# Performance work log

Hardware: AMD Instinct MI355X
Metric: run time of the kernel (lower is better)

The kernel has to match this reference:

```python
import jax, jax.numpy as jnp
import numpy as np

H_IMG, W_IMG = 1024, 1280
MAX_ITER = 3
DAMPING = 1e-6
DIST_THR = 0.2
NORM_THR = float(np.cos(np.deg2rad(20.0)))


def setup_inputs() -> dict:
    key = jax.random.key(0)
    k1, k2, k3, k4 = jax.random.split(key, 4)
    H, W = H_IMG, W_IMG
    fx = fy = 1000.0
    cx, cy = (W - 1) / 2.0, (H - 1) / 2.0
    K = jnp.array([[fx, 0.0, cx], [0.0, fy, cy], [0.0, 0.0, 1.0]], dtype=jnp.float32)
    # backproject a random depth map so vertex maps are geometrically consistent with K
    depth = 0.5 + 2.5 * jax.random.uniform(k1, (H, W), dtype=jnp.float32)
    vv, uu = jnp.meshgrid(jnp.arange(H, dtype=jnp.float32), jnp.arange(W, dtype=jnp.float32), indexing='ij')
    vertex_t0 = jnp.stack([(uu - cx) / fx * depth, (vv - cy) / fy * depth, depth], axis=-1)
    n = jax.random.normal(k2, (H, W, 3), dtype=jnp.float32) * 0.1 + jnp.array([0.0, 0.0, -1.0], jnp.float32)
    normal_t0 = n / jnp.linalg.norm(n, axis=-1, keepdims=True)
    # frame 1 = slightly perturbed frame 0 (realistic small-motion ICP)
    vertex_t1 = vertex_t0 + 0.002 * jax.random.normal(k3, (H, W, 3), dtype=jnp.float32)
    n1 = normal_t0 + 0.01 * jax.random.normal(k4, (H, W, 3), dtype=jnp.float32)
    normal_t1 = n1 / jnp.linalg.norm(n1, axis=-1, keepdims=True)
    pose10 = jnp.eye(4, dtype=jnp.float32).at[:3, 3].set(jnp.array([0.005, -0.003, 0.002], jnp.float32))
    return {
        'pose10': pose10,
        'vertex_t0': vertex_t0.astype(jnp.float32),
        'vertex_t1': vertex_t1.astype(jnp.float32),
        'normal_t0': normal_t0.astype(jnp.float32),
        'normal_t1': normal_t1.astype(jnp.float32),
        'K': K,
    }


def _skew3(w):
    o = jnp.zeros((), w.dtype)
    return jnp.array([[o, -w[2], w[1]], [w[2], o, -w[0]], [-w[1], w[0], o]])


def _exp_se3(xi):
    w, v = xi[:3], xi[3:6]
    wh = _skew3(w)
    wh2 = wh @ wh
    theta = jnp.linalg.norm(w)
    eps = 1e-8
    ts = jnp.maximum(theta, eps)  # safe denominator
    sin_t, cos_t = jnp.sin(ts), jnp.cos(ts)
    eye3 = jnp.eye(3, dtype=xi.dtype)
    e_w_big = eye3 + wh * (sin_t / ts) + wh2 * ((1.0 - cos_t) / ts ** 2)
    j_big = eye3 + ((1.0 - cos_t) / ts ** 2) * wh + ((ts - sin_t) / ts ** 3) * wh2
    small = theta <= eps
    e_w = jnp.where(small, eye3, e_w_big)
    j = jnp.where(small, eye3, j_big)
    return jnp.eye(4, dtype=xi.dtype).at[:3, :3].set(e_w).at[:3, 3].set(j @ v)


def _warp_nearest(feat, u, v):
    # grid_sample(mode='nearest', padding='border', align_corners=True) with
    # the module's normalization reduces to nearest-pixel gather at (v,u), clamped.
    H, W, _ = feat.shape
    ui = jnp.clip(jnp.round(u), 0, W - 1).astype(jnp.int32)
    vi = jnp.clip(jnp.round(v), 0, H - 1).astype(jnp.int32)
    return feat[vi, ui]  # (H,W,C)


def _icp_step(pose, vertex0, vertex1, normal0, normal1, mask0, K):
    R, t = pose[:3, :3], pose[:3, 3]
    H, W, _ = vertex0.shape
    p = vertex0 @ R.T + t          # vertex0_to1, (H,W,3)
    n0 = normal0 @ R.T             # normal0_to1
    fx, fy, cx, cy = K[0, 0], K[1, 1], K[0, 2], K[1, 2]
    z = p[..., 2]
    u = p[..., 0] / z * fx + cx
    v = p[..., 1] / z * fy + cy
    inview = (u > 0) & (u < W - 1) & (v > 0) & (v < H - 1)
    rv1 = _warp_nearest(vertex1, u, v)
    rn1 = _warp_nearest(normal1, u, v)
    mask1 = rv1[..., -1] > 0.0
    diff = p - rv1
    normal_ok = jnp.sum(n0 * rn1, axis=-1) > NORM_THR
    res = jnp.sum(rn1 * diff, axis=-1)           # (H,W)
    # -n^T skew(p) == cross(p, n)
    J = jnp.concatenate([jnp.cross(p, rn1), rn1], axis=-1)  # (H,W,6)
    occ = (~inview) | (jnp.linalg.norm(diff, axis=-1) > DIST_THR)
    invalid = occ | (~mask0) | (~mask1) | (~normal_ok)
    J = jnp.where(invalid[..., None], 0.0, J).reshape(-1, 6)
    r = jnp.where(invalid, 0.0, res).reshape(-1)
    JtJ = J.T @ J                                 # (6,6)
    JtR = J.T @ r                                 # (6,)
    Hm = JtJ + jnp.trace(JtJ) * DAMPING * jnp.eye(6, dtype=JtJ.dtype)
    xi = -(jnp.linalg.inv(Hm) @ JtR)
    return _exp_se3(xi) @ pose, ~invalid


def reference(pose10, vertex_t0, vertex_t1, normal_t0, normal_t1, K):
    mask0 = vertex_t0[..., -1] > 0.0
    pose = pose10
    valid = None
    for _ in range(MAX_ITER):
        pose, valid = _icp_step(pose, vertex_t0, vertex_t1, normal_t0, normal_t1, mask0, K)
    H, W = vertex_t0.shape[:2]
    valid_ratio = valid.astype(jnp.float32).sum() / H / W
    return pose, valid_ratio
```

## Files before the change

### kernel.cpp

```cpp
#include <hip/hip_runtime.h>
#include <math.h>

#define H_IMG 1024
#define W_IMG 1280
#define NPIX (H_IMG * W_IMG)
#define NQUAD (NPIX / 4)
#define RBLOCKS 256
#define RTPB 256
#define QPT (NQUAD / (RBLOCKS * RTPB))
#define NACC 28
#define NREP 8
#define NORM_THR 0.93969262f
#define DIST_THR2 0.04f
#define DAMPING 1e-6

#define ACC_DOUBLES (NREP * NACC * 8)

__global__ __launch_bounds__(256) void icp_init(const float* __restrict__ pose_in,
                                                double* __restrict__ ws) {
    const int i = threadIdx.x;
    if (i < 16) ws[i] = (double)pose_in[i];
    for (int k = i; k < ACC_DOUBLES; k += 256) ws[16 + k] = 0.0;
    if (i == 0) *(unsigned*)(ws + 16 + ACC_DOUBLES) = 0u;
}

__device__ void solve_and_update(const double* tot, double* pose_ws,
                                 float* out, int write_out) {
    double JtJ[6][6];
    {
        int k = 0;
        for (int i = 0; i < 6; ++i)
            for (int j = i; j < 6; ++j) { JtJ[i][j] = tot[k]; JtJ[j][i] = tot[k]; ++k; }
    }
    double tr = 0.0;
    for (int i = 0; i < 6; ++i) tr += JtJ[i][i];

    double A[6][7];
    for (int i = 0; i < 6; ++i) {
        for (int j = 0; j < 6; ++j) A[i][j] = JtJ[i][j] + (i == j ? tr * DAMPING : 0.0);
        A[i][6] = -tot[21 + i];
    }
    for (int c = 0; c < 6; ++c) {
        int piv = c; double mx = fabs(A[c][c]);
        for (int r = c + 1; r < 6; ++r) {
            double ar = fabs(A[r][c]);
            if (ar > mx) { mx = ar; piv = r; }
        }
        if (piv != c) for (int j = 0; j < 7; ++j) { double tmp = A[c][j]; A[c][j] = A[piv][j]; A[piv][j] = tmp; }
        double d = A[c][c]; if (d == 0.0) d = 1e-30;
        for (int r = c + 1; r < 6; ++r) {
            double f = A[r][c] / d;
            for (int j = c; j < 7; ++j) A[r][j] -= f * A[c][j];
        }
    }
    double xi[6];
    for (int i = 5; i >= 0; --i) {
        double s = A[i][6];
        for (int j = i + 1; j < 6; ++j) s -= A[i][j] * xi[j];
        double d = A[i][i]; if (d == 0.0) d = 1e-30;
        xi[i] = s / d;
    }

    const double w0 = xi[0], w1 = xi[1], w2 = xi[2];
    const double v0 = xi[3], v1 = xi[4], v2 = xi[5];
    double wh[3][3] = { {0.0, -w2, w1}, {w2, 0.0, -w0}, {-w1, w0, 0.0} };
    double wh2[3][3];
    for (int i = 0; i < 3; ++i)
        for (int j = 0; j < 3; ++j) {
            double s = 0.0;
            for (int k = 0; k < 3; ++k) s += wh[i][k] * wh[k][j];
            wh2[i][j] = s;
        }
    const double theta = sqrt(w0 * w0 + w1 * w1 + w2 * w2);
    const double eps = 1e-8;
    const double ts = (theta > eps) ? theta : eps;
    const double st = sin(ts), ct = cos(ts);
    const double cA = st / ts;
    const double cB = (1.0 - ct) / (ts * ts);
    const double cC = (ts - st) / (ts * ts * ts);
    const bool small = (theta <= eps);

    double ew[3][3], Jm[3][3];
    for (int i = 0; i < 3; ++i)
        for (int j = 0; j < 3; ++j) {
            double eye = (i == j) ? 1.0 : 0.0;
            ew[i][j] = small ? eye : (eye + cA * wh[i][j] + cB * wh2[i][j]);
            Jm[i][j] = small ? eye : (eye + cB * wh[i][j] + cC * wh2[i][j]);
        }
    double Jv[3];
    for (int i = 0; i < 3; ++i) Jv[i] = Jm[i][0] * v0 + Jm[i][1] * v1 + Jm[i][2] * v2;

    double T[16] = { ew[0][0], ew[0][1], ew[0][2], Jv[0],
                     ew[1][0], ew[1][1], ew[1][2], Jv[1],
                     ew[2][0], ew[2][1], ew[2][2], Jv[2],
                     0.0, 0.0, 0.0, 1.0 };
    double P[16];
    for (int i = 0; i < 16; ++i) P[i] = pose_ws[i];
    double NP[16];
    for (int i = 0; i < 4; ++i)
        for (int j = 0; j < 4; ++j) {
            double s = 0.0;
            for (int k = 0; k < 4; ++k) s += T[i * 4 + k] * P[k * 4 + j];
            NP[i * 4 + j] = s;
        }
    for (int i = 0; i < 16; ++i) pose_ws[i] = NP[i];

    if (write_out) {
        for (int i = 0; i < 16; ++i) out[i] = (float)NP[i];
        out[16] = (float)(tot[27] / (double)NPIX);
    }
}

__global__ __launch_bounds__(RTPB) void icp_fused(
    const float* __restrict__ vert0, const float* __restrict__ vert1,
    const float* __restrict__ norm0, const float* __restrict__ norm1,
    const float* __restrict__ Kmat, double* __restrict__ ws,
    float* __restrict__ out, int write_out)
{
    const double* pose = ws;
    double* acc = ws + 16;
    unsigned* counter = (unsigned*)(ws + 16 + ACC_DOUBLES);

    const float R00 = (float)pose[0],  R01 = (float)pose[1],  R02 = (float)pose[2],  t0 = (float)pose[3];
    const float R10 = (float)pose[4],  R11 = (float)pose[5],  R12 = (float)pose[6],  t1 = (float)pose[7];
    const float R20 = (float)pose[8],  R21 = (float)pose[9],  R22 = (float)pose[10], t2 = (float)pose[11];
    const float fx = Kmat[0], cx = Kmat[2], fy = Kmat[4], cy = Kmat[5];

    float a[NACC];
#pragma unroll
    for (int k = 0; k < NACC; ++k) a[k] = 0.0f;

    auto do_pixel = [&](float v0x, float v0y, float v0z,
                        float n0x, float n0y, float n0z) {
        const float px = R00 * v0x + R01 * v0y + R02 * v0z + t0;
        const float py = R10 * v0x + R11 * v0y + R12 * v0z + t1;
        const float pz = R20 * v0x + R21 * v0y + R22 * v0z + t2;
        const float nrx = R00 * n0x + R01 * n0y + R02 * n0z;
        const float nry = R10 * n0x + R11 * n0y + R12 * n0z;
        const float nrz = R20 * n0x + R21 * n0y + R22 * n0z;

        const float u = px / pz * fx + cx;
        const float v = py / pz * fy + cy;
        const bool inview = (u > 0.0f) && (u < (float)(W_IMG - 1)) &&
                            (v > 0.0f) && (v < (float)(H_IMG - 1));

        const float uf = fminf(fmaxf(rintf(u), 0.0f), (float)(W_IMG - 1));
        const float vf = fminf(fmaxf(rintf(v), 0.0f), (float)(H_IMG - 1));
        const int wbase = ((int)vf * W_IMG + (int)uf) * 3;

        const float r1x = vert1[wbase], r1y = vert1[wbase + 1], r1z = vert1[wbase + 2];
        const float m1x = norm1[wbase], m1y = norm1[wbase + 1], m1z = norm1[wbase + 2];

        const float dx = px - r1x, dy = py - r1y, dz = pz - r1z;
        const bool mask0 = v0z > 0.0f;
        const bool mask1 = r1z > 0.0f;
        const bool normal_ok = (nrx * m1x + nry * m1y + nrz * m1z) > NORM_THR;
        const float d2 = dx * dx + dy * dy + dz * dz;
        const bool occ = (!inview) || (d2 > DIST_THR2);
        const bool valid = (!occ) && mask0 && mask1 && normal_ok;

        if (valid) {
            const float res = m1x * dx + m1y * dy + m1z * dz;
            float J[6];
            J[0] = py * m1z - pz * m1y;
            J[1] = pz * m1x - px * m1z;
            J[2] = px * m1y - py * m1x;
            J[3] = m1x; J[4] = m1y; J[5] = m1z;
            int k = 0;
#pragma unroll
            for (int i = 0; i < 6; ++i)
#pragma unroll
                for (int j = i; j < 6; ++j) a[k++] += J[i] * J[j];
#pragma unroll
            for (int i = 0; i < 6; ++i) a[21 + i] += J[i] * res;
            a[27] += 1.0f;
        }
    };

    const int tid0 = blockIdx.x * RTPB + threadIdx.x;
    const float4* v0q = (const float4*)vert0;
    const float4* n0q = (const float4*)norm0;

#pragma unroll
    for (int i = 0; i < QPT; ++i) {
        const int q = tid0 + i * (RBLOCKS * RTPB);
        const float4 A0 = v0q[q * 3 + 0], A1 = v0q[q * 3 + 1], A2 = v0q[q * 3 + 2];
        const float4 B0 = n0q[q * 3 + 0], B1 = n0q[q * 3 + 1], B2 = n0q[q * 3 + 2];
        do_pixel(A0.x, A0.y, A0.z, B0.x, B0.y, B0.z);
        do_pixel(A0.w, A1.x, A1.y, B0.w, B1.x, B1.y);
        do_pixel(A1.z, A1.w, A2.x, B1.z, B1.w, B2.x);
        do_pixel(A2.y, A2.z, A2.w, B2.y, B2.z, B2.w);
    }

#pragma unroll
    for (int k = 0; k < NACC; ++k) {
        float val = a[k];
        for (int off = 32; off > 0; off >>= 1) val += __shfl_down(val, off, 64);
        a[k] = val;
    }

    __shared__ float sh[4][NACC];
    const int lane = threadIdx.x & 63;
    const int wid  = threadIdx.x >> 6;
    if (lane == 0) {
#pragma unroll
        for (int k = 0; k < NACC; ++k) sh[wid][k] = a[k];
    }
    __syncthreads();

    const unsigned tid = threadIdx.x;
    const int rep = blockIdx.x & (NREP - 1);
    if (tid < NACC) {
        double s = (double)sh[0][tid] + (double)sh[1][tid] +
                   (double)sh[2][tid] + (double)sh[3][tid];
        atomicAdd(&acc[(rep * NACC + (int)tid) * 8], s);
        __threadfence();
    }
    __syncthreads();

    __shared__ bool amLast;
    if (tid == 0) {
        unsigned prev = atomicAdd(counter, 1u);
        amLast = (prev == gridDim.x - 1);
    }
    __syncthreads();

    if (amLast) {
        __shared__ double tot[NACC];
        if (tid < NACC) {
            double s = 0.0;
            for (int r = 0; r < NREP; ++r)
                s += atomicAdd(&acc[(r * NACC + (int)tid) * 8], 0.0);
            tot[tid] = s;
            for (int r = 0; r < NREP; ++r)
                atomicExch((unsigned long long*)&acc[(r * NACC + (int)tid) * 8], 0ull);
        }
        if (tid == 0) atomicExch(counter, 0u);
        __syncthreads();
        if (tid == 0) solve_and_update(tot, ws, out, write_out);
    }
}

extern "C" void kernel_launch(void* const* d_in, const int* in_sizes, int n_in,
                              void* d_out, int out_size, void* d_ws, size_t ws_size,
                              hipStream_t stream) {
    const float* pose10 = (const float*)d_in[0];
    const float* vert0  = (const float*)d_in[1];
    const float* vert1  = (const float*)d_in[2];
    const float* norm0  = (const float*)d_in[3];
    const float* norm1  = (const float*)d_in[4];
    const float* Kmat   = (const float*)d_in[5];
    float* out = (float*)d_out;
    double* ws = (double*)d_ws;

    icp_init<<<1, 256, 0, stream>>>(pose10, ws);
    for (int it = 0; it < 3; ++it) {
        icp_fused<<<RBLOCKS, RTPB, 0, stream>>>(vert0, vert1, norm0, norm1,
                                                Kmat, ws, out, it == 2 ? 1 : 0);
    }
}
```

Measured before the change: 194.4 us.

## Prefetch next quad and batch gathers; replace atomic accumulators with per-block partials

The per-pixel loop now handles four pixels at a time. It computes all projections first, then issues all gather loads, and prefetches the next quad's vertex and normal data so memory latency overlaps with the accumulation math. The contended double atomicAdds into 8 replicas are replaced by per-block partial stores. The last block then reduces those partials in parallel, using 224 threads followed by a shared-memory tree step. This trades more register pressure (launch_bounds min-blocks set to 1) for more memory-level parallelism and fewer global atomics.

```diff
diff --git a/kernel.cpp b/kernel.cpp
--- a/kernel.cpp
+++ b/kernel.cpp
@@ -9,19 +9,18 @@
 #define RTPB 256
 #define QPT (NQUAD / (RBLOCKS * RTPB))
 #define NACC 28
-#define NREP 8
 #define NORM_THR 0.93969262f
 #define DIST_THR2 0.04f
 #define DAMPING 1e-6
 
-#define ACC_DOUBLES (NREP * NACC * 8)
+#define PART_DOUBLES (RBLOCKS * NACC)
 
 __global__ __launch_bounds__(256) void icp_init(const float* __restrict__ pose_in,
                                                 double* __restrict__ ws) {
     const int i = threadIdx.x;
     if (i < 16) ws[i] = (double)pose_in[i];
-    for (int k = i; k < ACC_DOUBLES; k += 256) ws[16 + k] = 0.0;
-    if (i == 0) *(unsigned*)(ws + 16 + ACC_DOUBLES) = 0u;
+    for (int k = i; k < PART_DOUBLES; k += 256) ws[16 + k] = 0.0;
+    if (i == 0) *(unsigned*)(ws + 16 + PART_DOUBLES) = 0u;
 }
 
 __device__ void solve_and_update(const double* tot, double* pose_ws,
@@ -111,15 +110,15 @@
     }
 }
 
-__global__ __launch_bounds__(RTPB) void icp_fused(
+__global__ __launch_bounds__(RTPB, 1) void icp_fused(
     const float* __restrict__ vert0, const float* __restrict__ vert1,
     const float* __restrict__ norm0, const float* __restrict__ norm1,
     const float* __restrict__ Kmat, double* __restrict__ ws,
     float* __restrict__ out, int write_out)
 {
     const double* pose = ws;
-    double* acc = ws + 16;
-    unsigned* counter = (unsigned*)(ws + 16 + ACC_DOUBLES);
+    double* part = ws + 16;
+    unsigned* counter = (unsigned*)(ws + 16 + PART_DOUBLES);
 
     const float R00 = (float)pose[0],  R01 = (float)pose[1],  R02 = (float)pose[2],  t0 = (float)pose[3];
     const float R10 = (float)pose[4],  R11 = (float)pose[5],  R12 = (float)pose[6],  t1 = (float)pose[7];
@@ -130,66 +129,93 @@
 #pragma unroll
     for (int k = 0; k < NACC; ++k) a[k] = 0.0f;
 
-    auto do_pixel = [&](float v0x, float v0y, float v0z,
-                        float n0x, float n0y, float n0z) {
-        const float px = R00 * v0x + R01 * v0y + R02 * v0z + t0;
-        const float py = R10 * v0x + R11 * v0y + R12 * v0z + t1;
-        const float pz = R20 * v0x + R21 * v0y + R22 * v0z + t2;
-        const float nrx = R00 * n0x + R01 * n0y + R02 * n0z;
-        const float nry = R10 * n0x + R11 * n0y + R12 * n0z;
-        const float nrz = R20 * n0x + R21 * n0y + R22 * n0z;
-
-        const float u = px / pz * fx + cx;
-        const float v = py / pz * fy + cy;
-        const bool inview = (u > 0.0f) && (u < (float)(W_IMG - 1)) &&
-                            (v > 0.0f) && (v < (float)(H_IMG - 1));
-
-        const float uf = fminf(fmaxf(rintf(u), 0.0f), (float)(W_IMG - 1));
-        const float vf = fminf(fmaxf(rintf(v), 0.0f), (float)(H_IMG - 1));
-        const int wbase = ((int)vf * W_IMG + (int)uf) * 3;
-
-        const float r1x = vert1[wbase], r1y = vert1[wbase + 1], r1z = vert1[wbase + 2];
-        const float m1x = norm1[wbase], m1y = norm1[wbase + 1], m1z = norm1[wbase + 2];
-
-        const float dx = px - r1x, dy = py - r1y, dz = pz - r1z;
-        const bool mask0 = v0z > 0.0f;
-        const bool mask1 = r1z > 0.0f;
-        const bool normal_ok = (nrx * m1x + nry * m1y + nrz * m1z) > NORM_THR;
-        const float d2 = dx * dx + dy * dy + dz * dz;
-        const bool occ = (!inview) || (d2 > DIST_THR2);
-        const bool valid = (!occ) && mask0 && mask1 && normal_ok;
-
-        if (valid) {
-            const float res = m1x * dx + m1y * dy + m1z * dz;
-            float J[6];
-            J[0] = py * m1z - pz * m1y;
-            J[1] = pz * m1x - px * m1z;
-            J[2] = px * m1y - py * m1x;
-            J[3] = m1x; J[4] = m1y; J[5] = m1z;
-            int k = 0;
-#pragma unroll
-            for (int i = 0; i < 6; ++i)
-#pragma unroll
-                for (int j = i; j < 6; ++j) a[k++] += J[i] * J[j];
-#pragma unroll
-            for (int i = 0; i < 6; ++i) a[21 + i] += J[i] * res;
-            a[27] += 1.0f;
-        }
-    };
-
     const int tid0 = blockIdx.x * RTPB + threadIdx.x;
     const float4* v0q = (const float4*)vert0;
     const float4* n0q = (const float4*)norm0;
 
+    float4 cA0, cA1, cA2, cB0, cB1, cB2;
+    {
+        const int q = tid0;
+        cA0 = v0q[q * 3 + 0]; cA1 = v0q[q * 3 + 1]; cA2 = v0q[q * 3 + 2];
+        cB0 = n0q[q * 3 + 0]; cB1 = n0q[q * 3 + 1]; cB2 = n0q[q * 3 + 2];
+    }
+
 #pragma unroll
     for (int i = 0; i < QPT; ++i) {
-        const int q = tid0 + i * (RBLOCKS * RTPB);
-        const float4 A0 = v0q[q * 3 + 0], A1 = v0q[q * 3 + 1], A2 = v0q[q * 3 + 2];
-        const float4 B0 = n0q[q * 3 + 0], B1 = n0q[q * 3 + 1], B2 = n0q[q * 3 + 2];
-        do_pixel(A0.x, A0.y, A0.z, B0.x, B0.y, B0.z);
-        do_pixel(A0.w, A1.x, A1.y, B0.w, B1.x, B1.y);
-        do_pixel(A1.z, A1.w, A2.x, B1.z, B1.w, B2.x);
-        do_pixel(A2.y, A2.z, A2.w, B2.y, B2.z, B2.w);
+        const float vx[4] = {cA0.x, cA0.w, cA1.z, cA2.y};
+        const float vy[4] = {cA0.y, cA1.x, cA1.w, cA2.z};
+        const float vz[4] = {cA0.z, cA1.y, cA2.x, cA2.w};
+        const float nx[4] = {cB0.x, cB0.w, cB1.z, cB2.y};
+        const float ny[4] = {cB0.y, cB1.x, cB1.w, cB2.z};
+        const float nz[4] = {cB0.z, cB1.y, cB2.x, cB2.w};
+
+        float px[4], py[4], pz[4], nrx[4], nry[4], nrz[4];
+        bool inview[4];
+        int wb[4];
+#pragma unroll
+        for (int p = 0; p < 4; ++p) {
+            px[p] = R00 * vx[p] + R01 * vy[p] + R02 * vz[p] + t0;
+            py[p] = R10 * vx[p] + R11 * vy[p] + R12 * vz[p] + t1;
+            pz[p] = R20 * vx[p] + R21 * vy[p] + R22 * vz[p] + t2;
+            nrx[p] = R00 * nx[p] + R01 * ny[p] + R02 * nz[p];
+            nry[p] = R10 * nx[p] + R11 * ny[p] + R12 * nz[p];
+            nrz[p] = R20 * nx[p] + R21 * ny[p] + R22 * nz[p];
+            const float u = px[p] / pz[p] * fx + cx;
+            const float v = py[p] / pz[p] * fy + cy;
+            inview[p] = (u > 0.0f) && (u < (float)(W_IMG - 1)) &&
+                        (v > 0.0f) && (v < (float)(H_IMG - 1));
+            const float uf = fminf(fmaxf(rintf(u), 0.0f), (float)(W_IMG - 1));
+            const float vf = fminf(fmaxf(rintf(v), 0.0f), (float)(H_IMG - 1));
+            wb[p] = ((int)vf * W_IMG + (int)uf) * 3;
+        }
+
+        float r1x[4], r1y[4], r1z[4], m1x[4], m1y[4], m1z[4];
+#pragma unroll
+        for (int p = 0; p < 4; ++p) {
+            r1x[p] = vert1[wb[p]]; r1y[p] = vert1[wb[p] + 1]; r1z[p] = vert1[wb[p] + 2];
+            m1x[p] = norm1[wb[p]]; m1y[p] = norm1[wb[p] + 1]; m1z[p] = norm1[wb[p] + 2];
+        }
+
+        float4 nA0, nA1, nA2, nB0, nB1, nB2;
+        if (i + 1 < QPT) {
+            const int q = tid0 + (i + 1) * (RBLOCKS * RTPB);
+            nA0 = v0q[q * 3 + 0]; nA1 = v0q[q * 3 + 1]; nA2 = v0q[q * 3 + 2];
+            nB0 = n0q[q * 3 + 0]; nB1 = n0q[q * 3 + 1]; nB2 = n0q[q * 3 + 2];
+        }
+
+#pragma unroll
+        for (int p = 0; p < 4; ++p) {
+            const float dx = px[p] - r1x[p], dy = py[p] - r1y[p], dz = pz[p] - r1z[p];
+            const bool mask0 = vz[p] > 0.0f;
+            const bool mask1 = r1z[p] > 0.0f;
+            const bool normal_ok =
+                (nrx[p] * m1x[p] + nry[p] * m1y[p] + nrz[p] * m1z[p]) > NORM_THR;
+            const float d2 = dx * dx + dy * dy + dz * dz;
+            const bool occ = (!inview[p]) || (d2 > DIST_THR2);
+            const bool valid = (!occ) && mask0 && mask1 && normal_ok;
+
+            if (valid) {
+                const float res = m1x[p] * dx + m1y[p] * dy + m1z[p] * dz;
+                float J[6];
+                J[0] = py[p] * m1z[p] - pz[p] * m1y[p];
+                J[1] = pz[p] * m1x[p] - px[p] * m1z[p];
+                J[2] = px[p] * m1y[p] - py[p] * m1x[p];
+                J[3] = m1x[p]; J[4] = m1y[p]; J[5] = m1z[p];
+                int k = 0;
+#pragma unroll
+                for (int ii = 0; ii < 6; ++ii)
+#pragma unroll
+                    for (int jj = ii; jj < 6; ++jj) a[k++] += J[ii] * J[jj];
+#pragma unroll
+                for (int ii = 0; ii < 6; ++ii) a[21 + ii] += J[ii] * res;
+                a[27] += 1.0f;
+            }
+        }
+
+        if (i + 1 < QPT) {
+            cA0 = nA0; cA1 = nA1; cA2 = nA2;
+            cB0 = nB0; cB1 = nB1; cB2 = nB2;
+        }
     }
 
 #pragma unroll
@@ -209,35 +235,50 @@
     __syncthreads();
 
     const unsigned tid = threadIdx.x;
-    const int rep = blockIdx.x & (NREP - 1);
     if (tid < NACC) {
         double s = (double)sh[0][tid] + (double)sh[1][tid] +
                    (double)sh[2][tid] + (double)sh[3][tid];
-        atomicAdd(&acc[(rep * NACC + (int)tid) * 8], s);
-        __threadfence();
+        __hip_atomic_store(&part[blockIdx.x * NACC + (int)tid], s,
+                           __ATOMIC_RELAXED, __HIP_MEMORY_SCOPE_AGENT);
     }
     __syncthreads();
 
     __shared__ bool amLast;
     if (tid == 0) {
+        __threadfence();
         unsigned prev = atomicAdd(counter, 1u);
         amLast = (prev == gridDim.x - 1);
     }
     __syncthreads();
 
     if (amLast) {
+        __threadfence();
+        __shared__ double red[8][NACC];
         __shared__ double tot[NACC];
+        const int k = (int)tid % NACC;
+        const int g = (int)tid / NACC;
+        if (tid < 8 * NACC) {
+            double s = 0.0;
+#pragma unroll
+            for (int b = 0; b < RBLOCKS / 8; ++b) {
+                const int blk = g + b * 8;
+                s += __hip_atomic_load(&part[blk * NACC + k],
+                                       __ATOMIC_RELAXED, __HIP_MEMORY_SCOPE_AGENT);
+            }
+            red[g][k] = s;
+        }
+        __syncthreads();
         if (tid < NACC) {
             double s = 0.0;
-            for (int r = 0; r < NREP; ++r)
-                s += atomicAdd(&acc[(r * NACC + (int)tid) * 8], 0.0);
+#pragma unroll
+            for (int g2 = 0; g2 < 8; ++g2) s += red[g2][tid];
             tot[tid] = s;
-            for (int r = 0; r < NREP; ++r)
-                atomicExch((unsigned long long*)&acc[(r * NACC + (int)tid) * 8], 0ull);
-        }
-        if (tid == 0) atomicExch(counter, 0u);
+        }
         __syncthreads();
-        if (tid == 0) solve_and_update(tot, ws, out, write_out);
+        if (tid == 0) {
+            solve_and_update(tot, ws, out, write_out);
+            atomicExch(counter, 0u);
+        }
     }
 }
 
```

Result: slower. 209.9 us (+8.0%).
